# Kernel tuning notes

Hardware: AMD Instinct MI355X
Metric: run time of the kernel (lower is better)

Reference implementation:

```python
import jax, jax.numpy as jnp
import numpy as np

C = 128   # c_pair
N = 512   # num residues (pair grid side)
OUTGOING = True
EPS = 1e-5


def _layernorm(x, w, b):
    m = jnp.mean(x, axis=-1, keepdims=True)
    v = jnp.var(x, axis=-1, keepdims=True)
    return (x - m) * jax.lax.rsqrt(v + EPS) * w + b


def setup_inputs() -> dict:
    key = jax.random.key(0)
    ks = jax.random.split(key, 8)
    s = 1.0 / np.sqrt(C)
    return {
        "act": jax.random.normal(ks[0], (N, N, C), jnp.float32),
        "mask": (jax.random.uniform(ks[1], (N, N)) > 0.1).astype(jnp.float32),
        "ln_in_w": jnp.ones((C,), jnp.float32),
        "ln_in_b": jnp.zeros((C,), jnp.float32),
        "W_proj": jax.random.normal(ks[2], (2 * C, C), jnp.float32) * s,
        "W_gate": jax.random.normal(ks[3], (2 * C, C), jnp.float32) * s,
        "ln_c_w": jnp.ones((C,), jnp.float32),
        "ln_c_b": jnp.zeros((C,), jnp.float32),
        "W_out": jax.random.normal(ks[4], (C, C), jnp.float32) * s,
        "W_glin": jax.random.normal(ks[5], (C, C), jnp.float32) * s,
    }


def reference(act, mask, ln_in_w, ln_in_b, W_proj, W_gate, ln_c_w, ln_c_b, W_out, W_glin):
    # left input layernorm
    x = _layernorm(act, ln_in_w, ln_in_b)                       # [N,N,C]
    # masked, sigmoid-gated projection to 2C channels
    p = jnp.einsum('ijc,dc->ijd', x, W_proj)                    # [N,N,2C]
    p = p * mask[..., None]
    p = p * jax.nn.sigmoid(jnp.einsum('ijc,dc->ijd', x, W_gate))
    a, b = p[..., :C], p[..., C:]
    # triangle einsum (channel-first 'cik,cjk->cij' or 'ckj,cki->cij',
    # written channel-last here)
    if OUTGOING:
        t = jnp.einsum('ikc,jkc->ijc', a, b)                    # [N,N,C]
    else:
        t = jnp.einsum('kjc,kic->ijc', a, b)
    # center norm + output projection, gated by sigmoid of normalized input
    t = _layernorm(t, ln_c_w, ln_c_b)
    out = jnp.einsum('ijc,dc->ijd', t, W_out)
    out = out * jax.nn.sigmoid(jnp.einsum('ijc,dc->ijd', x, W_glin))
    return out
```

## Files before the change

### kernel.cpp

```cpp
#include <hip/hip_runtime.h>


#define NN 512
#define CC 128
#define NPOS (NN * NN)
#define LN_EPS 1e-5f

typedef __attribute__((ext_vector_type(8))) short bf16x8;
typedef __attribute__((ext_vector_type(4))) float f32x4;

__device__ __forceinline__ float bitf(unsigned int u) {
    return __builtin_bit_cast(float, u);
}
__device__ __forceinline__ float b2f(unsigned short u) {
    return bitf(((unsigned int)u) << 16);
}
__device__ __forceinline__ unsigned short f2b(float f) {
    unsigned int u = __builtin_bit_cast(unsigned int, f);
    u = u + 0x7FFFu + ((u >> 16) & 1u);
    return (unsigned short)(u >> 16);
}
__device__ __forceinline__ float sigmoidf(float x) {
    return 1.0f / (1.0f + __expf(-x));
}

__global__ __launch_bounds__(256) void k_ln_proj(
    const float* __restrict__ act, const float* __restrict__ mask,
    const float* __restrict__ lw, const float* __restrict__ lb,
    const float* __restrict__ Wproj, const float* __restrict__ Wgate,
    const float* __restrict__ Wglin,
    unsigned short* __restrict__ a_ws, unsigned short* __restrict__ b_ws,
    unsigned short* __restrict__ g_ws)
{
    __shared__ __align__(16) unsigned short Xs[128 * 136];
    __shared__ __align__(16) float WL[4352];
    unsigned short* Wu = (unsigned short*)WL;

    const int tid = threadIdx.x;
    const int m0 = blockIdx.x * 128;

    {
        const int c4 = tid & 31;
        float4 w4 = *(const float4*)(lw + c4 * 4);
        float4 b4 = *(const float4*)(lb + c4 * 4);
        for (int it = 0; it < 16; ++it) {
            int p = (tid >> 5) + it * 8;
            float4 v = *(const float4*)(act + (size_t)(m0 + p) * CC + c4 * 4);
            float s  = v.x + v.y + v.z + v.w;
            float ss = v.x * v.x + v.y * v.y + v.z * v.z + v.w * v.w;
            #pragma unroll
            for (int ofs = 1; ofs < 32; ofs <<= 1) {
                s  += __shfl_xor(s, ofs);
                ss += __shfl_xor(ss, ofs);
            }
            float mean = s * (1.0f / 128.0f);
            float var  = ss * (1.0f / 128.0f) - mean * mean;
            float rstd = rsqrtf(var + LN_EPS);
            ushort4 o;
            o.x = f2b((v.x - mean) * rstd * w4.x + b4.x);
            o.y = f2b((v.y - mean) * rstd * w4.y + b4.y);
            o.z = f2b((v.z - mean) * rstd * w4.z + b4.z);
            o.w = f2b((v.w - mean) * rstd * w4.w + b4.w);
            *(ushort4*)&Xs[p * 136 + c4 * 4] = o;
        }
    }

    const int lane  = tid & 63;
    const int wid   = tid >> 6;
    const int row16 = lane & 15, kg = lane >> 4;
    const int wrm = (wid >> 1) * 64;
    const int wcn = (wid & 1) * 32;

    for (int chunk = 0; chunk < 10; ++chunk) {
        __syncthreads();
        {
            int r = tid >> 2, q = tid & 3;
            const float* wrow;
            if (chunk < 8) {
                int d = chunk * 32 + (r >> 1);
                wrow = (r & 1) ? (Wgate + d * CC) : (Wproj + d * CC);
            } else {
                wrow = Wglin + ((chunk - 8) * 64 + r) * CC;
            }
            #pragma unroll
            for (int t = 0; t < 8; ++t) {
                float4 v = *(const float4*)(wrow + q * 32 + t * 4);
                ushort4 o;
                o.x = f2b(v.x); o.y = f2b(v.y); o.z = f2b(v.z); o.w = f2b(v.w);
                *(ushort4*)&Wu[r * 136 + q * 32 + t * 4] = o;
            }
        }
        __syncthreads();

        f32x4 acc[4][2] = {};
        #pragma unroll
        for (int ks = 0; ks < 4; ++ks) {
            const int koff = ks * 32 + kg * 8;
            bf16x8 xa[4], wb[2];
            #pragma unroll
            for (int mf = 0; mf < 4; ++mf)
                xa[mf] = *(const bf16x8*)&Xs[(wrm + mf * 16 + row16) * 136 + koff];
            #pragma unroll
            for (int nf = 0; nf < 2; ++nf)
                wb[nf] = *(const bf16x8*)&Wu[(wcn + nf * 16 + row16) * 136 + koff];
            #pragma unroll
            for (int mf = 0; mf < 4; ++mf)
                #pragma unroll
                for (int nf = 0; nf < 2; ++nf)
                    acc[mf][nf] = __builtin_amdgcn_mfma_f32_16x16x32_bf16(
                        xa[mf], wb[nf], acc[mf][nf], 0, 0, 0);
        }

        for (int h = 0; h < 2; ++h) {
            __syncthreads();
            if ((wid >> 1) == h) {
                #pragma unroll
                for (int nf = 0; nf < 2; ++nf) {
                    #pragma unroll
                    for (int mf = 0; mf < 4; ++mf) {
                        int r = wcn + nf * 16 + row16;
                        int mloc = mf * 16 + kg * 4;
                        float* dst = &WL[r * 66 + mloc];
                        f32x4 v = acc[mf][nf];
                        *(float2*)(dst)     = make_float2(v.x, v.y);
                        *(float2*)(dst + 2) = make_float2(v.z, v.w);
                    }
                }
            }
            __syncthreads();
            if (chunk < 8) {
                int dd = tid >> 3, mseg = tid & 7;
                float4 p0 = *(const float4*)&WL[(2 * dd) * 66 + mseg * 8];
                float4 p1 = *(const float4*)&WL[(2 * dd) * 66 + mseg * 8 + 4];
                float4 g0 = *(const float4*)&WL[(2 * dd + 1) * 66 + mseg * 8];
                float4 g1 = *(const float4*)&WL[(2 * dd + 1) * 66 + mseg * 8 + 4];
                const float* mkp = mask + m0 + h * 64 + mseg * 8;
                float4 mk0 = *(const float4*)(mkp);
                float4 mk1 = *(const float4*)(mkp + 4);
                unsigned short ob[8];
                ob[0] = f2b(p0.x * mk0.x * sigmoidf(g0.x));
                ob[1] = f2b(p0.y * mk0.y * sigmoidf(g0.y));
                ob[2] = f2b(p0.z * mk0.z * sigmoidf(g0.z));
                ob[3] = f2b(p0.w * mk0.w * sigmoidf(g0.w));
                ob[4] = f2b(p1.x * mk1.x * sigmoidf(g1.x));
                ob[5] = f2b(p1.y * mk1.y * sigmoidf(g1.y));
                ob[6] = f2b(p1.z * mk1.z * sigmoidf(g1.z));
                ob[7] = f2b(p1.w * mk1.w * sigmoidf(g1.w));
                unsigned short* plane = (chunk < 4) ? a_ws : b_ws;
                int D = (chunk & 3) * 32 + dd;
                uint4 w;
                w.x = (unsigned)ob[0] | ((unsigned)ob[1] << 16);
                w.y = (unsigned)ob[2] | ((unsigned)ob[3] << 16);
                w.z = (unsigned)ob[4] | ((unsigned)ob[5] << 16);
                w.w = (unsigned)ob[6] | ((unsigned)ob[7] << 16);
                *(uint4*)(plane + (size_t)D * NPOS + m0 + h * 64 + mseg * 8) = w;
            } else {
                int mm = tid >> 2, q = tid & 3;
                unsigned short ob[16];
                #pragma unroll
                for (int rr = 0; rr < 16; ++rr)
                    ob[rr] = f2b(sigmoidf(WL[(q * 16 + rr) * 66 + mm]));
                uint4 w0, w1;
                w0.x = (unsigned)ob[0]  | ((unsigned)ob[1]  << 16);
                w0.y = (unsigned)ob[2]  | ((unsigned)ob[3]  << 16);
                w0.z = (unsigned)ob[4]  | ((unsigned)ob[5]  << 16);
                w0.w = (unsigned)ob[6]  | ((unsigned)ob[7]  << 16);
                w1.x = (unsigned)ob[8]  | ((unsigned)ob[9]  << 16);
                w1.y = (unsigned)ob[10] | ((unsigned)ob[11] << 16);
                w1.z = (unsigned)ob[12] | ((unsigned)ob[13] << 16);
                w1.w = (unsigned)ob[14] | ((unsigned)ob[15] << 16);
                unsigned short* gp = g_ws + (size_t)(m0 + h * 64 + mm) * CC +
                                     (chunk - 8) * 64 + q * 16;
                *(uint4*)gp = w0;
                *(uint4*)(gp + 8) = w1;
            }
        }
    }
}

__global__ __launch_bounds__(256) void k_tri(
    const unsigned short* __restrict__ a_ws,
    const unsigned short* __restrict__ b_ws,
    unsigned short* __restrict__ t_ws)
{
    __shared__ __align__(16) unsigned short As[8192];
    __shared__ __align__(16) unsigned short Bs[8192];

    const int tid  = threadIdx.x;
    const int lane = tid & 63;
    const int wid  = tid >> 6;
    const int c    = blockIdx.y;
    const int i0   = (blockIdx.x >> 2) * 128;
    const int j0   = (blockIdx.x & 3) * 128;

    const size_t plane = (size_t)c * NPOS;
    const unsigned short* Ag = a_ws + plane + (size_t)i0 * NN;
    const unsigned short* Bg = b_ws + plane + (size_t)j0 * NN;

    const int row16 = lane & 15, kg = lane >> 4;
    const int wrm = (wid >> 1) * 64;
    const int wcn = (wid & 1) * 64;
    const int xr  = (lane & 7) << 4;

    int srcOff[4];
    #pragma unroll
    for (int q = 0; q < 4; ++q) {
        int p  = (wid * 4 + q) * 1024 + lane * 16;
        int lg = p ^ (((p >> 7) & 7) << 4);
        int r = lg >> 7, k16 = (lg >> 4) & 7;
        srcOff[q] = r * NN + k16 * 8;
    }

    f32x4 acc[4][4] = {};

    for (int kt = 0; kt < 8; ++kt) {
        const int k0 = kt * 64;
        __syncthreads();
        #pragma unroll
        for (int q = 0; q < 4; ++q) {
            int ldsOff = (wid * 4 + q) * 512;
            __builtin_amdgcn_global_load_lds(
                (const __attribute__((address_space(1))) void*)(Ag + srcOff[q] + k0),
                (__attribute__((address_space(3))) void*)(As + ldsOff), 16, 0, 0);
            __builtin_amdgcn_global_load_lds(
                (const __attribute__((address_space(1))) void*)(Bg + srcOff[q] + k0),
                (__attribute__((address_space(3))) void*)(Bs + ldsOff), 16, 0, 0);
        }
        __syncthreads();

        #pragma unroll
        for (int ks = 0; ks < 2; ++ks) {
            const int kb = ks * 64 + kg * 16;
            bf16x8 af[4], bfr[4];
            #pragma unroll
            for (int mf = 0; mf < 4; ++mf) {
                int lA = ((wrm + mf * 16 + row16) << 7) + kb;
                af[mf] = *(const bf16x8*)((const char*)As + (lA ^ xr));
            }
            #pragma unroll
            for (int nf = 0; nf < 4; ++nf) {
                int lB = ((wcn + nf * 16 + row16) << 7) + kb;
                bfr[nf] = *(const bf16x8*)((const char*)Bs + (lB ^ xr));
            }
            #pragma unroll
            for (int mf = 0; mf < 4; ++mf)
                #pragma unroll
                for (int nf = 0; nf < 4; ++nf)
                    acc[mf][nf] = __builtin_amdgcn_mfma_f32_16x16x32_bf16(
                        af[mf], bfr[nf], acc[mf][nf], 0, 0, 0);
        }
    }

    unsigned short* tp = t_ws + plane;
    #pragma unroll
    for (int mf = 0; mf < 4; ++mf) {
        int i = i0 + wrm + mf * 16 + kg * 4;
        #pragma unroll
        for (int nf = 0; nf < 4; ++nf) {
            int j = j0 + wcn + nf * 16 + row16;
            f32x4 v = acc[mf][nf];
            tp[(size_t)(i + 0) * NN + j] = f2b(v.x);
            tp[(size_t)(i + 1) * NN + j] = f2b(v.y);
            tp[(size_t)(i + 2) * NN + j] = f2b(v.z);
            tp[(size_t)(i + 3) * NN + j] = f2b(v.w);
        }
    }
}

__global__ __launch_bounds__(256) void k_ln_out(
    const unsigned short* __restrict__ t_ws,
    const unsigned short* __restrict__ g_ws,
    const float* __restrict__ lw, const float* __restrict__ lb,
    const float* __restrict__ Wout,
    float* __restrict__ out)
{
    __shared__ float X[64 * 132];
    __shared__ unsigned short W[64 * 132];

    const int tid = threadIdx.x;
    const int m0 = blockIdx.x * 64;

    for (int it = 0; it < 8; ++it) {
        int c  = it * 16 + (tid >> 4);
        int mm = (tid & 15) * 4;
        ushort4 u = *(const ushort4*)(t_ws + (size_t)c * NPOS + m0 + mm);
        X[(mm + 0) * 132 + c] = b2f(u.x);
        X[(mm + 1) * 132 + c] = b2f(u.y);
        X[(mm + 2) * 132 + c] = b2f(u.z);
        X[(mm + 3) * 132 + c] = b2f(u.w);
    }
    __syncthreads();

    {
        int p = tid >> 2, q = tid & 3;
        float s = 0.f, ss = 0.f;
        #pragma unroll
        for (int t = 0; t < 32; ++t) {
            float v = X[p * 132 + q * 32 + t];
            s += v; ss += v * v;
        }
        s += __shfl_xor(s, 1); ss += __shfl_xor(ss, 1);
        s += __shfl_xor(s, 2); ss += __shfl_xor(ss, 2);
        float mean = s * (1.0f / 128.0f);
        float var  = ss * (1.0f / 128.0f) - mean * mean;
        float rstd = rsqrtf(var + LN_EPS);
        #pragma unroll
        for (int t = 0; t < 32; ++t) {
            int c = q * 32 + t;
            float v = X[p * 132 + c];
            X[p * 132 + c] = (v - mean) * rstd * lw[c] + lb[c];
        }
    }

    const int tx = tid & 15, ty = tid >> 4;

    for (int chunk = 0; chunk < 2; ++chunk) {
        __syncthreads();
        for (int idx = tid; idx < 64 * 32; idx += 256) {
            int r = idx >> 5, k4 = idx & 31;
            const float* wrow = Wout + (chunk * 64 + r) * CC;
            float4 v = *(const float4*)(wrow + k4 * 4);
            unsigned short* dst = &W[r * 132 + k4 * 4];
            dst[0] = f2b(v.x); dst[1] = f2b(v.y);
            dst[2] = f2b(v.z); dst[3] = f2b(v.w);
        }
        __syncthreads();

        float acc[4][4] = {};
        for (int k = 0; k < 128; k += 4) {
            float4 xr[4];
            #pragma unroll
            for (int pp = 0; pp < 4; ++pp)
                xr[pp] = *(const float4*)&X[(ty * 4 + pp) * 132 + k];
            #pragma unroll
            for (int dd = 0; dd < 4; ++dd) {
                const unsigned short* wp = &W[(tx * 4 + dd) * 132 + k];
                float w0 = b2f(wp[0]), w1 = b2f(wp[1]);
                float w2 = b2f(wp[2]), w3 = b2f(wp[3]);
                #pragma unroll
                for (int pp = 0; pp < 4; ++pp)
                    acc[pp][dd] += xr[pp].x * w0 + xr[pp].y * w1 +
                                   xr[pp].z * w2 + xr[pp].w * w3;
            }
        }

        #pragma unroll
        for (int pp = 0; pp < 4; ++pp) {
            int m = m0 + ty * 4 + pp;
            int d0 = chunk * 64 + tx * 4;
            const unsigned short* gp = g_ws + (size_t)m * CC + d0;
            float4 o;
            o.x = acc[pp][0] * b2f(gp[0]);
            o.y = acc[pp][1] * b2f(gp[1]);
            o.z = acc[pp][2] * b2f(gp[2]);
            o.w = acc[pp][3] * b2f(gp[3]);
            *(float4*)(out + (size_t)m * CC + d0) = o;
        }
    }
}

extern "C" void kernel_launch(void* const* d_in, const int* in_sizes, int n_in,
                              void* d_out, int out_size, void* d_ws, size_t ws_size,
                              hipStream_t stream) {
    const float* act   = (const float*)d_in[0];
    const float* mask  = (const float*)d_in[1];
    const float* lnw   = (const float*)d_in[2];
    const float* lnb   = (const float*)d_in[3];
    const float* Wproj = (const float*)d_in[4];
    const float* Wgate = (const float*)d_in[5];
    const float* lncw  = (const float*)d_in[6];
    const float* lncb  = (const float*)d_in[7];
    const float* Wout  = (const float*)d_in[8];
    const float* Wglin = (const float*)d_in[9];
    float* out = (float*)d_out;

    char* ws = (char*)d_ws;
    unsigned short* a_ws = (unsigned short*)(ws);
    unsigned short* b_ws = (unsigned short*)(ws + 67108864);
    unsigned short* g_ws = (unsigned short*)(ws + 134217728);
    unsigned short* t_ws = (unsigned short*)(ws + 201326592);

    k_ln_proj<<<dim3(2048), dim3(256), 0, stream>>>(
        act, mask, lnw, lnb, Wproj, Wgate, Wglin, a_ws, b_ws, g_ws);

    k_tri<<<dim3(16, 128), dim3(256), 0, stream>>>(a_ws, b_ws, t_ws);

    k_ln_out<<<dim3(4096), dim3(256), 0, stream>>>(
        t_ws, g_ws, lncw, lncb, Wout, out);
}
```

Before: 651.9 us.

## Restructure output kernel with channel-major LDS tile and transposed weights

Rewrites the final LN+output-projection kernel to store the normalized tile channel-major in LDS and load the whole transposed W_out once, instead of in two chunks. Global reads of t use 16-byte loads, and the inner product becomes an outer-product loop with a 4x8 register tile per thread, with vectorized loads of the gate and stores of the output. This is meant to cut LDS bank conflicts, redundant barriers and scalar bf16 conversions, at the cost of more LDS per block and more registers. The transposed weight stores into LDS are scattered 2-byte writes.

```diff
diff --git a/kernel.cpp b/kernel.cpp
--- a/kernel.cpp
+++ b/kernel.cpp
@@ -22,6 +22,12 @@
 }
 __device__ __forceinline__ float sigmoidf(float x) {
     return 1.0f / (1.0f + __expf(-x));
+}
+__device__ __forceinline__ void unpack8(uint4 u, float* dst) {
+    dst[0] = bitf(u.x << 16); dst[1] = bitf(u.x & 0xFFFF0000u);
+    dst[2] = bitf(u.y << 16); dst[3] = bitf(u.y & 0xFFFF0000u);
+    dst[4] = bitf(u.z << 16); dst[5] = bitf(u.z & 0xFFFF0000u);
+    dst[6] = bitf(u.w << 16); dst[7] = bitf(u.w & 0xFFFF0000u);
 }
 
 __global__ __launch_bounds__(256) void k_ln_proj(
@@ -267,36 +273,48 @@
     }
 }
 
-__global__ __launch_bounds__(256) void k_ln_out(
-    const unsigned short* __restrict__ t_ws,
+__global__ __launch_bounds__(256) void k_out(
+    const unsigned short* __restrict__ tT,
     const unsigned short* __restrict__ g_ws,
     const float* __restrict__ lw, const float* __restrict__ lb,
     const float* __restrict__ Wout,
     float* __restrict__ out)
 {
-    __shared__ float X[64 * 132];
-    __shared__ unsigned short W[64 * 132];
+    __shared__ __align__(16) float Xf[128 * 68];
+    __shared__ __align__(16) unsigned short Wt[128 * 132];
 
     const int tid = threadIdx.x;
     const int m0 = blockIdx.x * 64;
 
-    for (int it = 0; it < 8; ++it) {
-        int c  = it * 16 + (tid >> 4);
-        int mm = (tid & 15) * 4;
-        ushort4 u = *(const ushort4*)(t_ws + (size_t)c * NPOS + m0 + mm);
-        X[(mm + 0) * 132 + c] = b2f(u.x);
-        X[(mm + 1) * 132 + c] = b2f(u.y);
-        X[(mm + 2) * 132 + c] = b2f(u.z);
-        X[(mm + 3) * 132 + c] = b2f(u.w);
+    #pragma unroll
+    for (int it = 0; it < 4; ++it) {
+        int c  = (tid >> 3) + it * 32;
+        int mg = tid & 7;
+        uint4 u = *(const uint4*)(tT + (size_t)c * NPOS + m0 + mg * 8);
+        float f[8];
+        unpack8(u, f);
+        float* dst = &Xf[c * 68 + mg * 8];
+        #pragma unroll
+        for (int t = 0; t < 8; ++t) dst[t] = f[t];
+    }
+    #pragma unroll
+    for (int it = 0; it < 16; ++it) {
+        int idx = tid + it * 256;
+        int d = idx >> 5, c4 = idx & 31;
+        float4 v = *(const float4*)(Wout + d * CC + c4 * 4);
+        Wt[(c4 * 4 + 0) * 132 + d] = f2b(v.x);
+        Wt[(c4 * 4 + 1) * 132 + d] = f2b(v.y);
+        Wt[(c4 * 4 + 2) * 132 + d] = f2b(v.z);
+        Wt[(c4 * 4 + 3) * 132 + d] = f2b(v.w);
     }
     __syncthreads();
 
     {
-        int p = tid >> 2, q = tid & 3;
+        int m = tid >> 2, q = tid & 3;
         float s = 0.f, ss = 0.f;
         #pragma unroll
         for (int t = 0; t < 32; ++t) {
-            float v = X[p * 132 + q * 32 + t];
+            float v = Xf[(q * 32 + t) * 68 + m];
             s += v; ss += v * v;
         }
         s += __shfl_xor(s, 1); ss += __shfl_xor(ss, 1);
@@ -307,55 +325,50 @@
         #pragma unroll
         for (int t = 0; t < 32; ++t) {
             int c = q * 32 + t;
-            float v = X[p * 132 + c];
-            X[p * 132 + c] = (v - mean) * rstd * lw[c] + lb[c];
-        }
-    }
+            float v = Xf[c * 68 + m];
+            Xf[c * 68 + m] = (v - mean) * rstd * lw[c] + lb[c];
+        }
+    }
+    __syncthreads();
 
     const int tx = tid & 15, ty = tid >> 4;
-
-    for (int chunk = 0; chunk < 2; ++chunk) {
-        __syncthreads();
-        for (int idx = tid; idx < 64 * 32; idx += 256) {
-            int r = idx >> 5, k4 = idx & 31;
-            const float* wrow = Wout + (chunk * 64 + r) * CC;
-            float4 v = *(const float4*)(wrow + k4 * 4);
-            unsigned short* dst = &W[r * 132 + k4 * 4];
-            dst[0] = f2b(v.x); dst[1] = f2b(v.y);
-            dst[2] = f2b(v.z); dst[3] = f2b(v.w);
-        }
-        __syncthreads();
-
-        float acc[4][4] = {};
-        for (int k = 0; k < 128; k += 4) {
-            float4 xr[4];
-            #pragma unroll
-            for (int pp = 0; pp < 4; ++pp)
-                xr[pp] = *(const float4*)&X[(ty * 4 + pp) * 132 + k];
-            #pragma unroll
-            for (int dd = 0; dd < 4; ++dd) {
-                const unsigned short* wp = &W[(tx * 4 + dd) * 132 + k];
-                float w0 = b2f(wp[0]), w1 = b2f(wp[1]);
-                float w2 = b2f(wp[2]), w3 = b2f(wp[3]);
-                #pragma unroll
-                for (int pp = 0; pp < 4; ++pp)
-                    acc[pp][dd] += xr[pp].x * w0 + xr[pp].y * w1 +
-                                   xr[pp].z * w2 + xr[pp].w * w3;
-            }
-        }
-
-        #pragma unroll
-        for (int pp = 0; pp < 4; ++pp) {
-            int m = m0 + ty * 4 + pp;
-            int d0 = chunk * 64 + tx * 4;
-            const unsigned short* gp = g_ws + (size_t)m * CC + d0;
-            float4 o;
-            o.x = acc[pp][0] * b2f(gp[0]);
-            o.y = acc[pp][1] * b2f(gp[1]);
-            o.z = acc[pp][2] * b2f(gp[2]);
-            o.w = acc[pp][3] * b2f(gp[3]);
-            *(float4*)(out + (size_t)m * CC + d0) = o;
-        }
+    float acc[4][8] = {};
+    #pragma unroll 4
+    for (int c = 0; c < 128; ++c) {
+        float4 xv = *(const float4*)&Xf[c * 68 + ty * 4];
+        const unsigned short* wp = &Wt[c * 132 + tx * 8];
+        uint2 wa = *(const uint2*)(wp);
+        uint2 wbu = *(const uint2*)(wp + 4);
+        float w[8];
+        w[0] = bitf(wa.x << 16);  w[1] = bitf(wa.x & 0xFFFF0000u);
+        w[2] = bitf(wa.y << 16);  w[3] = bitf(wa.y & 0xFFFF0000u);
+        w[4] = bitf(wbu.x << 16); w[5] = bitf(wbu.x & 0xFFFF0000u);
+        w[6] = bitf(wbu.y << 16); w[7] = bitf(wbu.y & 0xFFFF0000u);
+        float xr[4] = {xv.x, xv.y, xv.z, xv.w};
+        #pragma unroll
+        for (int i2 = 0; i2 < 4; ++i2)
+            #pragma unroll
+            for (int j = 0; j < 8; ++j)
+                acc[i2][j] += xr[i2] * w[j];
+    }
+
+    #pragma unroll
+    for (int i2 = 0; i2 < 4; ++i2) {
+        int m = m0 + ty * 4 + i2;
+        const unsigned short* gp = g_ws + (size_t)m * CC + tx * 8;
+        ushort4 ga = *(const ushort4*)(gp);
+        ushort4 gb = *(const ushort4*)(gp + 4);
+        float4 o0, o1;
+        o0.x = acc[i2][0] * b2f(ga.x);
+        o0.y = acc[i2][1] * b2f(ga.y);
+        o0.z = acc[i2][2] * b2f(ga.z);
+        o0.w = acc[i2][3] * b2f(ga.w);
+        o1.x = acc[i2][4] * b2f(gb.x);
+        o1.y = acc[i2][5] * b2f(gb.y);
+        o1.z = acc[i2][6] * b2f(gb.z);
+        o1.w = acc[i2][7] * b2f(gb.w);
+        *(float4*)(out + (size_t)m * CC + tx * 8) = o0;
+        *(float4*)(out + (size_t)m * CC + tx * 8 + 4) = o1;
     }
 }
 
@@ -385,6 +398,6 @@
 
     k_tri<<<dim3(16, 128), dim3(256), 0, stream>>>(a_ws, b_ws, t_ws);
 
-    k_ln_out<<<dim3(4096), dim3(256), 0, stream>>>(
+    k_out<<<dim3(4096), dim3(256), 0, stream>>>(
         t_ws, g_ws, lncw, lncb, Wout, out);
 }
```

Result: faster. 607.3 us (-6.8%).
